# Kernel tuning notes

Measured on AMD Instinct MI355X. Metric: run time of the kernel, lower is better.

## Reference

```python
import jax, jax.numpy as jnp
import numpy as np

M, NN, D, H, DFF, L, EPG = 128, 62, 512, 8, 2048, 4, 600
K1, K2 = 50, 40  # ceil(0.8*62), ceil(0.8*50)
EPS = 1e-5


def _ln(x, g, b):
    mu = x.mean(-1, keepdims=True)
    v = x.var(-1, keepdims=True)
    return (x - mu) * jax.lax.rsqrt(v + EPS) * g + b


def _gcn(x, src, dst, mask, W, b, n):
    # PyG GCNConv: add self-loops, sym-normalized scatter-add aggregation
    h = x @ W
    w = mask.astype(x.dtype)
    deg = 1.0 + jax.ops.segment_sum(w, dst, num_segments=n)  # +1 self-loop
    dis = jax.lax.rsqrt(deg)
    coef = dis[src] * w * dis[dst]
    agg = jax.ops.segment_sum(coef[:, None] * h[src], dst, num_segments=n)
    return agg + h * (dis * dis)[:, None] + b  # second term = self-loop message


def _sagpool(x, src, dst, mask, Ws, bs, m, n_per, k):
    n = m * n_per
    score = _gcn(x, src, dst, mask, Ws, bs, n)[:, 0]
    _, topi = jax.lax.top_k(score.reshape(m, n_per), k)  # per-graph topk
    perm = (topi + jnp.arange(m)[:, None] * n_per).reshape(-1)
    xn = x[perm] * jnp.tanh(score[perm])[:, None]
    # filter_adj: keep edges with both endpoints surviving, remap indices
    nmap = jnp.full((n,), -1, jnp.int32).at[perm].set(jnp.arange(m * k, dtype=jnp.int32))
    ns, nd = nmap[src], nmap[dst]
    keep = mask & (ns >= 0) & (nd >= 0)
    return xn, jnp.where(keep, ns, 0), jnp.where(keep, nd, 0), keep


def _enc_layer(x, Wqkv, bqkv, Wo, bo, W1, b1, W2, b2, g1, be1, g2, be2):
    # post-norm TransformerEncoderLayer, relu activation, eval (no dropout)
    S, B, Dm = x.shape
    dh = Dm // H
    q, k, v = jnp.split(x @ Wqkv + bqkv, 3, axis=-1)
    q = q.reshape(S, B, H, dh)
    k = k.reshape(S, B, H, dh)
    v = v.reshape(S, B, H, dh)
    att = jnp.einsum('sbhd,tbhd->bhst', q, k) * (1.0 / np.sqrt(dh))
    o = jnp.einsum('bhst,tbhd->sbhd', jax.nn.softmax(att, axis=-1), v).reshape(S, B, Dm)
    x = _ln(x + o @ Wo + bo, g1, be1)
    f = jax.nn.relu(x @ W1 + b1) @ W2 + b2
    return _ln(x + f, g2, be2)


def _readout(h, m, k):
    hr = h.reshape(m, k, -1)
    return jnp.concatenate([hr.max(axis=1), hr.mean(axis=1)], axis=-1)  # gmp||gap


def _forward(edge_index, x, bn_g, bn_b, W_emb, enc_Wqkv, enc_bqkv, enc_Wo, enc_bo, enc_W1, enc_b1, enc_W2, enc_b2, enc_g1, enc_be1, enc_g2, enc_be2, W_emb1, conv1_W, conv1_b, convs_W, convs_b, pool1_W, pool1_b, pool2_W, pool2_b, fc1_W, fc1_b, fc2_W, fc2_b, fc3_W, fc3_b):
    m = x.shape[0] // NN
    xr = x.reshape(m, NN, NN)
    # BatchNorm1d(62) in training mode: per-channel stats over (N, L)
    mu = xr.mean(axis=(0, 2), keepdims=True)
    var = xr.var(axis=(0, 2), keepdims=True)
    xb = (xr - mu) * jax.lax.rsqrt(var + EPS) * bn_g[None, :, None] + bn_b[None, :, None]
    t = xb.transpose(1, 0, 2) @ W_emb  # [62, m, D] seq-first
    for l in range(L):
        t = _enc_layer(t, enc_Wqkv[l], enc_bqkv[l], enc_Wo[l], enc_bo[l], enc_W1[l], enc_b1[l], enc_W2[l], enc_b2[l], enc_g1[l], enc_be1[l], enc_g2[l], enc_be2[l])
    # faithful to torch: reshape [62,m,62] directly to [m*62,62] (no permute back)
    xg = (t @ W_emb1).reshape(m * NN, NN)
    src, dst = edge_index[0], edge_index[1]
    mask0 = jnp.ones(src.shape, bool)
    h = jax.nn.relu(_gcn(xg, src, dst, mask0, conv1_W, conv1_b, m * NN))
    h, s1, d1, m1 = _sagpool(h, src, dst, mask0, pool1_W, pool1_b, m, NN, K1)
    x1 = _readout(h, m, K1)
    for l in range(L - 1):
        h = jax.nn.relu(_gcn(h, s1, d1, m1, convs_W[l], convs_b[l], m * K1))
    h, s2, d2, m2 = _sagpool(h, s1, d1, m1, pool2_W, pool2_b, m, K1, K2)
    x2 = _readout(h, m, K2)
    z = x1 + x2
    z = jax.nn.relu(z @ fc1_W + fc1_b)
    z = jax.nn.relu(z @ fc2_W + fc2_b)
    return z @ fc3_W + fc3_b


def setup_inputs():
    key = jax.random.key(0)
    ki = iter(jax.random.split(key, 40))
    def nrm(shape, s=0.05):
        return jax.random.normal(next(ki), shape, jnp.float32) * s
    x = jax.random.normal(next(ki), (M * NN, NN), jnp.float32)
    off = jnp.arange(M, dtype=jnp.int32)[:, None] * NN
    src = jax.random.randint(next(ki), (M, EPG), 0, NN, dtype=jnp.int32) + off
    dst = jax.random.randint(next(ki), (M, EPG), 0, NN, dtype=jnp.int32) + off
    edge_index = jnp.stack([src.reshape(-1), dst.reshape(-1)])
    return dict(
        x=x, edge_index=edge_index,
        bn_g=jnp.ones(NN), bn_b=jnp.zeros(NN),
        W_emb=nrm((NN, D)),
        enc_Wqkv=nrm((L, D, 3 * D)), enc_bqkv=jnp.zeros((L, 3 * D)),
        enc_Wo=nrm((L, D, D)), enc_bo=jnp.zeros((L, D)),
        enc_W1=nrm((L, D, DFF)), enc_b1=jnp.zeros((L, DFF)),
        enc_W2=nrm((L, DFF, D)), enc_b2=jnp.zeros((L, D)),
        enc_g1=jnp.ones((L, D)), enc_be1=jnp.zeros((L, D)),
        enc_g2=jnp.ones((L, D)), enc_be2=jnp.zeros((L, D)),
        W_emb1=nrm((D, NN)),
        conv1_W=nrm((NN, D)), conv1_b=jnp.zeros(D),
        convs_W=nrm((L - 1, D, D)), convs_b=jnp.zeros((L - 1, D)),
        pool1_W=nrm((D, 1)), pool1_b=jnp.zeros(1),
        pool2_W=nrm((D, 1)), pool2_b=jnp.zeros(1),
        fc1_W=nrm((2 * D, D)), fc1_b=jnp.zeros(D),
        fc2_W=nrm((D, D // 2)), fc2_b=jnp.zeros(D // 2),
        fc3_W=nrm((D // 2, 2)), fc3_b=jnp.zeros(2))


def reference(x, edge_index, bn_g, bn_b, W_emb, enc_Wqkv, enc_bqkv, enc_Wo, enc_bo, enc_W1, enc_b1, enc_W2, enc_b2, enc_g1, enc_be1, enc_g2, enc_be2, W_emb1, conv1_W, conv1_b, convs_W, convs_b, pool1_W, pool1_b, pool2_W, pool2_b, fc1_W, fc1_b, fc2_W, fc2_b, fc3_W, fc3_b):
    return _forward(edge_index, x, bn_g, bn_b, W_emb, enc_Wqkv, enc_bqkv, enc_Wo, enc_bo, enc_W1, enc_b1, enc_W2, enc_b2, enc_g1, enc_be1, enc_g2, enc_be2, W_emb1, conv1_W, conv1_b, convs_W, convs_b, pool1_W, pool1_b, pool2_W, pool2_b, fc1_W, fc1_b, fc2_W, fc2_b, fc3_W, fc3_b)
```

## Files before the change

### kernel.cpp

```cpp
#include <hip/hip_runtime.h>
#include <float.h>
#include <math.h>

#define MG 128
#define NNODE 62
#define DD 512
#define NH 8
#define DH 64
#define DFF 2048
#define NLAYER 4
#define EPG 600
#define KP1 50
#define KP2 40
#define NTOK (MG*NNODE)
#define NEDGE (MG*EPG)
#define EPSV 1e-5f
#define PW 68

typedef unsigned short u16;
using bf16x8 = __attribute__((ext_vector_type(8))) short;
using f32x4  = __attribute__((ext_vector_type(4))) float;

__device__ __forceinline__ float wave_sum(float v) {
  for (int off = 32; off; off >>= 1) v += __shfl_xor(v, off);
  return v;
}
__device__ __forceinline__ float wave_max(float v) {
  for (int off = 32; off; off >>= 1) v = fmaxf(v, __shfl_xor(v, off));
  return v;
}
__device__ __forceinline__ u16 f2b(float x) {
  union { float f; unsigned u; } v; v.f = x;
  unsigned r = v.u + 0x7fffu + ((v.u >> 16) & 1u);
  return (u16)(r >> 16);
}
__device__ __forceinline__ float b2f(u16 h) {
  union { float f; unsigned u; } v; v.u = ((unsigned)h) << 16;
  return v.f;
}
__device__ __forceinline__ void f2bsplit(float x, u16& h, u16& l) {
  h = f2b(x);
  l = f2b(x - b2f(h));
}
__device__ __forceinline__ void load_lds16(const u16* g, u16* l) {
  __builtin_amdgcn_global_load_lds(
      (const __attribute__((address_space(1))) unsigned int*)(const void*)g,
      (__attribute__((address_space(3))) unsigned int*)(void*)l, 16, 0, 0);
}
__device__ __forceinline__ void cvt8(const float* __restrict__ p, bf16x8& vh, bf16x8& vl) {
  #pragma unroll
  for (int e = 0; e < 8; ++e) {
    u16 h, l; f2bsplit(p[e], h, l);
    vh[e] = (short)h; vl[e] = (short)l;
  }
}
__device__ __forceinline__ void cvt8s(const float* __restrict__ p, bf16x8& vh, bf16x8& vl) {
  #pragma unroll
  for (int e = 0; e < 8; ++e) {
    u16 h, l; f2bsplit(p[e*PW], h, l);
    vh[e] = (short)h; vl[e] = (short)l;
  }
}

__global__ __launch_bounds__(256) void bn_stats_kernel(const float* __restrict__ x,
    float* __restrict__ mu, float* __restrict__ rs) {
  int s = blockIdx.x;
  float sum = 0.f, sq = 0.f;
  for (int i = threadIdx.x; i < MG*NNODE; i += 256) {
    int b = i / NNODE, j = i - b*NNODE;
    float v = x[(size_t)(b*NNODE + s)*NNODE + j];
    sum += v; sq += v*v;
  }
  __shared__ float r1[4], r2[4];
  sum = wave_sum(sum); sq = wave_sum(sq);
  int wv = threadIdx.x >> 6, lane = threadIdx.x & 63;
  if (lane == 0) { r1[wv] = sum; r2[wv] = sq; }
  __syncthreads();
  if (threadIdx.x == 0) {
    float S = r1[0]+r1[1]+r1[2]+r1[3];
    float Q = r2[0]+r2[1]+r2[2]+r2[3];
    float m = S / (float)(MG*NNODE);
    float var = Q / (float)(MG*NNODE) - m*m;
    mu[s] = m;
    rs[s] = rsqrtf(var + EPSV);
  }
}

__global__ __launch_bounds__(256) void embed_kernel(const float* __restrict__ x,
    const float* __restrict__ mu, const float* __restrict__ rs,
    const float* __restrict__ gg, const float* __restrict__ bb,
    const float* __restrict__ W,
    u16* __restrict__ Th, u16* __restrict__ Tl) {
  int tok = blockIdx.x;
  int s = tok >> 7, b = tok & 127;
  __shared__ float xb[NNODE];
  if (threadIdx.x < NNODE) {
    float v = x[(size_t)(b*NNODE + s)*NNODE + threadIdx.x];
    xb[threadIdx.x] = (v - mu[s]) * rs[s] * gg[s] + bb[s];
  }
  __syncthreads();
  int d = threadIdx.x;
  float a0 = 0.f, a1 = 0.f;
  for (int j = 0; j < NNODE; ++j) {
    float xv = xb[j];
    a0 += xv * W[(size_t)j*DD + d];
    a1 += xv * W[(size_t)j*DD + d + 256];
  }
  size_t o = (size_t)tok*DD + d;
  u16 h, l;
  f2bsplit(a0, h, l); Th[o] = h; Tl[o] = l;
  f2bsplit(a1, h, l); Th[o+256] = h; Tl[o+256] = l;
}

__global__ __launch_bounds__(256) void gemm_kernel(const float* __restrict__ A,
    const float* __restrict__ B, float* __restrict__ C, int M, int N, int K) {
  __shared__ float As[16][68];
  __shared__ float Bs[16][68];
  int bm = blockIdx.y * 64, bn = blockIdx.x * 64;
  int tid = threadIdx.x;
  int tx = tid & 15, ty = tid >> 4;
  float acc[4][4] = {};
  for (int k0 = 0; k0 < K; k0 += 16) {
    {
      int row = tid >> 2; int kk = (tid & 3) * 4;
      int gm = bm + row;
      #pragma unroll
      for (int i = 0; i < 4; ++i) {
        int gk = k0 + kk + i;
        As[kk+i][row] = (gm < M && gk < K) ? A[(size_t)gm*K + gk] : 0.f;
      }
    }
    {
      int krow = tid >> 4; int nn = (tid & 15) * 4;
      int gk = k0 + krow;
      #pragma unroll
      for (int i = 0; i < 4; ++i) {
        int gn = bn + nn + i;
        Bs[krow][nn+i] = (gk < K && gn < N) ? B[(size_t)gk*N + gn] : 0.f;
      }
    }
    __syncthreads();
    #pragma unroll
    for (int k = 0; k < 16; ++k) {
      float a[4], bb2[4];
      #pragma unroll
      for (int i = 0; i < 4; ++i) a[i] = As[k][ty*4+i];
      #pragma unroll
      for (int j = 0; j < 4; ++j) bb2[j] = Bs[k][tx*4+j];
      #pragma unroll
      for (int i = 0; i < 4; ++i)
        #pragma unroll
        for (int j = 0; j < 4; ++j) acc[i][j] += a[i]*bb2[j];
    }
    __syncthreads();
  }
  #pragma unroll
  for (int i = 0; i < 4; ++i) {
    int gm = bm + ty*4 + i;
    if (gm >= M) continue;
    #pragma unroll
    for (int j = 0; j < 4; ++j) {
      int gn = bn + tx*4 + j;
      if (gn >= N) continue;
      C[(size_t)gm*N + gn] = acc[i][j];
    }
  }
}

__device__ __forceinline__ void transpose_split_tile(const float* __restrict__ W,
    u16* __restrict__ th, u16* __restrict__ tl,
    int K, int N, int Kp, int bx, int by, float (*t)[65]) {
  int k0 = by*64, n0 = bx*64;
  for (int i = threadIdx.x; i < 64*64; i += 256) {
    int r = i >> 6, c = i & 63;
    int gk = k0 + r, gn = n0 + c;
    t[r][c] = (gk < K && gn < N) ? W[(size_t)gk*N + gn] : 0.f;
  }
  __syncthreads();
  for (int i = threadIdx.x; i < 64*64; i += 256) {
    int r = i >> 6, c = i & 63;
    int gn = n0 + r, gk = k0 + c;
    u16 h, l; f2bsplit(t[c][r], h, l);
    th[(size_t)gn*Kp + gk] = h;
    tl[(size_t)gn*Kp + gk] = l;
  }
}

__global__ __launch_bounds__(256) void allT_kernel(
    const float* __restrict__ Wqkv, const float* __restrict__ Wo,
    const float* __restrict__ W1, const float* __restrict__ W2,
    u16* WQh, u16* WQl, u16* WOh, u16* WOl,
    u16* W1h, u16* W1l, u16* W2h, u16* W2l) {
  __shared__ float t[64][65];
  int layer = blockIdx.x / 768;
  int b = blockIdx.x % 768;
  const float* wqkv = Wqkv + (size_t)layer*DD*3*DD;
  const float* wo   = Wo   + (size_t)layer*DD*DD;
  const float* w1   = W1   + (size_t)layer*DD*DFF;
  const float* w2   = W2   + (size_t)layer*DFF*DD;
  size_t oq = (size_t)layer*1536*512, oo = (size_t)layer*512*512;
  size_t o1 = (size_t)layer*2048*512, o2 = (size_t)layer*512*2048;
  if (b < 192)      transpose_split_tile(wqkv, WQh+oq, WQl+oq, 512, 1536, 512, b % 24, b / 24, t);
  else if (b < 256) { int q = b - 192; transpose_split_tile(wo, WOh+oo, WOl+oo, 512, 512, 512, q % 8, q / 8, t); }
  else if (b < 512) { int q = b - 256; transpose_split_tile(w1, W1h+o1, W1l+o1, 512, 2048, 512, q % 32, q / 32, t); }
  else              { int q = b - 512; transpose_split_tile(w2, W2h+o2, W2l+o2, 2048, 512, 2048, q % 8, q / 8, t); }
}

__global__ __launch_bounds__(256) void gcnT_kernel(
    const float* __restrict__ WC, const float* __restrict__ convs_W,
    u16* CTh, u16* CTl, u16* CVh, u16* CVl) {
  __shared__ float t[64][65];
  int job = blockIdx.x >> 6, q = blockIdx.x & 63;
  int bx = q % 8, by = q / 8;
  if (job == 0) transpose_split_tile(WC, CTh, CTl, 512, 512, 512, bx, by, t);
  else {
    int l = job - 1;
    transpose_split_tile(convs_W + (size_t)l*DD*DD,
        CVh + (size_t)l*DD*DD, CVl + (size_t)l*DD*DD, 512, 512, 512, bx, by, t);
  }
}

template<bool RELU, int OUTMODE>
__global__ __launch_bounds__(256) void gemm3_kernel(
    const u16* __restrict__ Ah, const u16* __restrict__ Al,
    const u16* __restrict__ Bh, const u16* __restrict__ Bl,
    const float* __restrict__ bias,
    float* __restrict__ Cf, u16* __restrict__ Ch, u16* __restrict__ Cl,
    int Nreal, int Nstride, int Kp, int KC) {
  __shared__ alignas(16) u16 sA[2][2][4096];
  __shared__ alignas(16) u16 sB[2][2][4096];
  unsigned nx = gridDim.x, ny = gridDim.y;
  unsigned nwg = nx * ny * gridDim.z;
  unsigned lb = blockIdx.x + nx*(blockIdx.y + ny*blockIdx.z);
  unsigned swz = lb;
  if ((nwg & 7u) == 0u) {
    unsigned cpx = nwg >> 3;
    swz = (lb & 7u)*cpx + (lb >> 3);
  }
  unsigned bxi = swz % nx;
  unsigned rem = swz / nx;
  unsigned byi = rem % ny;
  unsigned bzi = rem / ny;
  int bm = byi * 128, bn = bxi * 128;
  int z = bzi;
  int tid = threadIdx.x;
  int wv = tid >> 6, lane = tid & 63;
  int wr = (wv >> 1) * 64, wc = (wv & 1) * 64;
  f32x4 acc[4][4];
  #pragma unroll
  for (int i = 0; i < 4; ++i)
    #pragma unroll
    for (int j = 0; j < 4; ++j) acc[i][j] = (f32x4){0.f,0.f,0.f,0.f};

  int r0 = tid >> 2;
  int lin = (tid & 3) * 8;
  int c0 = lin ^ (((r0 >> 1) & 3) << 3);
  int r1 = r0 + 64;
  int c1 = lin ^ (((r1 >> 1) & 3) << 3);
  int fr = lane & 15, fo = (lane >> 4) * 8;

  int kbeg = z * KC;
  const u16* pA0 = Ah + (size_t)(bm + r0)*Kp + kbeg + c0;
  const u16* pA1 = Ah + (size_t)(bm + r1)*Kp + kbeg + c1;
  const u16* pB0 = Bh + (size_t)(bn + r0)*Kp + kbeg + c0;
  const u16* pB1 = Bh + (size_t)(bn + r1)*Kp + kbeg + c1;
  const ptrdiff_t dA = Al - Ah;
  const ptrdiff_t dB = Bl - Bh;

  auto stage = [&](int bi) {
    load_lds16(pA0,      &sA[bi][0][tid*8]);
    load_lds16(pA1,      &sA[bi][0][2048 + tid*8]);
    load_lds16(pA0 + dA, &sA[bi][1][tid*8]);
    load_lds16(pA1 + dA, &sA[bi][1][2048 + tid*8]);
    load_lds16(pB0,      &sB[bi][0][tid*8]);
    load_lds16(pB1,      &sB[bi][0][2048 + tid*8]);
    load_lds16(pB0 + dB, &sB[bi][1][tid*8]);
    load_lds16(pB1 + dB, &sB[bi][1][2048 + tid*8]);
    pA0 += 32; pA1 += 32; pB0 += 32; pB1 += 32;
  };

  int nk = KC >> 5;
  stage(0);
  int cur = 0;
  for (int t = 0; t < nk; ++t) {
    if (t + 1 < nk) {
      stage(cur ^ 1);
      asm volatile("s_waitcnt vmcnt(8)" ::: "memory");
    } else {
      asm volatile("s_waitcnt vmcnt(0)" ::: "memory");
    }
    __builtin_amdgcn_s_barrier();
    __builtin_amdgcn_sched_barrier(0);
    bf16x8 ah[4], al[4], bh[4], bl[4];
    #pragma unroll
    for (int i = 0; i < 4; ++i) {
      int ra = wr + i*16 + fr;
      int ea = ra*32 + (fo ^ (((ra >> 1) & 3) << 3));
      ah[i] = *(const bf16x8*)&sA[cur][0][ea];
      al[i] = *(const bf16x8*)&sA[cur][1][ea];
      int rb = wc + i*16 + fr;
      int eb = rb*32 + (fo ^ (((rb >> 1) & 3) << 3));
      bh[i] = *(const bf16x8*)&sB[cur][0][eb];
      bl[i] = *(const bf16x8*)&sB[cur][1][eb];
    }
    #pragma unroll
    for (int i = 0; i < 4; ++i)
      #pragma unroll
      for (int j = 0; j < 4; ++j) {
        acc[i][j] = __builtin_amdgcn_mfma_f32_16x16x32_bf16(ah[i], bh[j], acc[i][j], 0, 0, 0);
        acc[i][j] = __builtin_amdgcn_mfma_f32_16x16x32_bf16(ah[i], bl[j], acc[i][j], 0, 0, 0);
        acc[i][j] = __builtin_amdgcn_mfma_f32_16x16x32_bf16(al[i], bh[j], acc[i][j], 0, 0, 0);
      }
    __builtin_amdgcn_s_barrier();
    cur ^= 1;
  }
  size_t pstride = (size_t)gridDim.y * 128 * Nstride;
  int cr = (lane >> 4) * 4, cc = lane & 15;
  #pragma unroll
  for (int i = 0; i < 4; ++i) {
    #pragma unroll
    for (int j = 0; j < 4; ++j) {
      int gn = bn + wc + j*16 + cc;
      if (gn >= Nstride) continue;
      #pragma unroll
      for (int q = 0; q < 4; ++q) {
        int gm = bm + wr + i*16 + cr + q;
        float v = acc[i][j][q];
        if (gn < Nreal) { if (bias && z == 0) v += bias[gn]; } else v = 0.f;
        if (RELU) v = fmaxf(v, 0.f);
        if (OUTMODE == 0) {
          Cf[(size_t)z*pstride + (size_t)gm*Nstride + gn] = v;
        } else if (OUTMODE == 1) {
          size_t o = (size_t)z*pstride + (size_t)gm*Nstride + gn;
          u16 h, l; f2bsplit(v, h, l);
          Ch[o] = h; Cl[o] = l;
        } else {
          int which = gn >> 9, hh2 = (gn >> 6) & 7, d = gn & 63;
          int b2 = gm & 127, s2 = gm >> 7;
          Cf[(size_t)((which*NH + hh2)*MG + b2)*4096 + s2*64 + d] = v;
        }
      }
    }
  }
}

__global__ __launch_bounds__(256) void attn_kernel(const float* __restrict__ QKV,
    u16* __restrict__ Oh, u16* __restrict__ Ol) {
  int b = blockIdx.x >> 3, h = blockIdx.x & 7;
  __shared__ float sQ[64*PW];
  __shared__ float sK[64*PW];
  __shared__ float sV[64*PW];
  u16* sPh = (u16*)sK;
  u16* sPl = ((u16*)sK) + 4096;
  float* Ss = sQ;
  int tid = threadIdx.x, wv = tid >> 6, lane = tid & 63;
  int fr = lane & 15, fq = lane >> 4;
  size_t base0 = (size_t)(h*MG + b)*4096;
  const float* Qg = QKV + base0;
  const float* Kg = QKV + (size_t)NH*MG*4096 + base0;
  const float* Vg = QKV + (size_t)2*NH*MG*4096 + base0;
  #pragma unroll
  for (int i = 0; i < 4; ++i) {
    int c = tid + i*256;
    int r = c >> 4, col = (c & 15) * 4;
    f32x4 q4 = *(const f32x4*)(Qg + (size_t)c*4);
    f32x4 k4 = *(const f32x4*)(Kg + (size_t)c*4);
    f32x4 v4 = *(const f32x4*)(Vg + (size_t)c*4);
    *(f32x4*)&sQ[r*PW + col] = q4;
    *(f32x4*)&sK[r*PW + col] = k4;
    *(f32x4*)&sV[r*PW + col] = v4;
  }
  if (tid < 128) sV[(62 + (tid >> 6))*PW + (tid & 63)] = 0.f;
  __syncthreads();
  int rA = 16*wv + fr;
  bf16x8 qh[2], ql[2];
  #pragma unroll
  for (int kk = 0; kk < 2; ++kk)
    cvt8(&sQ[rA*PW + 32*kk + 8*fq], qh[kk], ql[kk]);
  __syncthreads();
  f32x4 accS[4];
  #pragma unroll
  for (int j = 0; j < 4; ++j) accS[j] = (f32x4){0.f,0.f,0.f,0.f};
  __builtin_amdgcn_s_setprio(1);
  #pragma unroll
  for (int kk = 0; kk < 2; ++kk) {
    #pragma unroll
    for (int j = 0; j < 4; ++j) {
      int rB = 16*j + fr;
      bf16x8 kh, kl;
      cvt8(&sK[rB*PW + 32*kk + 8*fq], kh, kl);
      accS[j] = __builtin_amdgcn_mfma_f32_16x16x32_bf16(qh[kk], kh, accS[j], 0, 0, 0);
      accS[j] = __builtin_amdgcn_mfma_f32_16x16x32_bf16(qh[kk], kl, accS[j], 0, 0, 0);
      accS[j] = __builtin_amdgcn_mfma_f32_16x16x32_bf16(ql[kk], kh, accS[j], 0, 0, 0);
    }
  }
  __builtin_amdgcn_s_setprio(0);
  #pragma unroll
  for (int j = 0; j < 4; ++j)
    #pragma unroll
    for (int q = 0; q < 4; ++q)
      Ss[(16*wv + fq*4 + q)*PW + 16*j + fr] = accS[j][q];
  __syncthreads();
  for (int rr = 0; rr < 16; ++rr) {
    int row = 16*wv + rr;
    float sv = (lane < NNODE) ? Ss[row*PW + lane]*0.125f : -FLT_MAX;
    float mx = wave_max(sv);
    float e = (lane < NNODE) ? expf(sv - mx) : 0.f;
    float sm = wave_sum(e);
    float p = e / sm;
    u16 ph, pl; f2bsplit(p, ph, pl);
    int pos = row*64 + ((((lane >> 3) ^ (row & 7)) << 3) | (lane & 7));
    sPh[pos] = ph; sPl[pos] = pl;
  }
  __syncthreads();
  f32x4 accO[4];
  #pragma unroll
  for (int j = 0; j < 4; ++j) accO[j] = (f32x4){0.f,0.f,0.f,0.f};
  __builtin_amdgcn_s_setprio(1);
  #pragma unroll
  for (int kk = 0; kk < 2; ++kk) {
    int cha = (((4*kk + fq) ^ (rA & 7)) << 3);
    bf16x8 pah = *(const bf16x8*)&sPh[rA*64 + cha];
    bf16x8 pal = *(const bf16x8*)&sPl[rA*64 + cha];
    #pragma unroll
    for (int j = 0; j < 4; ++j) {
      bf16x8 vh, vl;
      cvt8s(&sV[(32*kk + 8*fq)*PW + 16*j + fr], vh, vl);
      accO[j] = __builtin_amdgcn_mfma_f32_16x16x32_bf16(pah, vh, accO[j], 0, 0, 0);
      accO[j] = __builtin_amdgcn_mfma_f32_16x16x32_bf16(pah, vl, accO[j], 0, 0, 0);
      accO[j] = __builtin_amdgcn_mfma_f32_16x16x32_bf16(pal, vh, accO[j], 0, 0, 0);
    }
  }
  __builtin_amdgcn_s_setprio(0);
  #pragma unroll
  for (int j = 0; j < 4; ++j) {
    #pragma unroll
    for (int q = 0; q < 4; ++q) {
      int s2 = 16*wv + fq*4 + q;
      if (s2 < NNODE) {
        int d = 16*j + fr;
        size_t o = ((size_t)(s2*MG + b))*DD + h*DH + d;
        u16 hh2, ll2; f2bsplit(accO[j][q], hh2, ll2);
        Oh[o] = hh2; Ol[o] = ll2;
      }
    }
  }
}

__global__ __launch_bounds__(256) void add_ln_kernel(
    u16* __restrict__ Xh, u16* __restrict__ Xl,
    const float* __restrict__ P, int nchunk,
    const float* __restrict__ gg, const float* __restrict__ bb) {
  size_t row = blockIdx.x;
  int t = threadIdx.x;
  const size_t MN = (size_t)NTOK*DD;
  float r0 = 0.f, r1 = 0.f;
  for (int z = 0; z < nchunk; ++z) {
    r0 += P[z*MN + row*DD + t];
    r1 += P[z*MN + row*DD + t + 256];
  }
  float v0 = b2f(Xh[row*DD + t]) + b2f(Xl[row*DD + t]) + r0;
  float v1 = b2f(Xh[row*DD + t + 256]) + b2f(Xl[row*DD + t + 256]) + r1;
  __shared__ float red[4];
  float s = wave_sum(v0 + v1);
  int wv = t >> 6, lane = t & 63;
  if (lane == 0) red[wv] = s;
  __syncthreads();
  float mu = (red[0]+red[1]+red[2]+red[3]) * (1.f/DD);
  float d0 = v0 - mu, d1 = v1 - mu;
  float q = wave_sum(d0*d0 + d1*d1);
  __syncthreads();
  if (lane == 0) red[wv] = q;
  __syncthreads();
  float var = (red[0]+red[1]+red[2]+red[3]) * (1.f/DD);
  float rs = rsqrtf(var + EPSV);
  float o0 = d0*rs*gg[t] + bb[t];
  float o1 = d1*rs*gg[t+256] + bb[t+256];
  u16 h, l;
  f2bsplit(o0, h, l); Xh[row*DD + t] = h; Xl[row*DD + t] = l;
  f2bsplit(o1, h, l); Xh[row*DD + t+256] = h; Xl[row*DD + t+256] = l;
}

__global__ void fill_int_kernel(int* p, int v, int n) {
  int i = blockIdx.x*256 + threadIdx.x;
  if (i < n) p[i] = v;
}
__global__ void zero_f_kernel(float* p, int n) {
  int i = blockIdx.x*256 + threadIdx.x;
  if (i < n) p[i] = 0.f;
}
__global__ void count_deg_kernel(const int* __restrict__ dst, int* deg, int n) {
  int e = blockIdx.x*256 + threadIdx.x;
  if (e < n) atomicAdd(&deg[dst[e]], 1);
}
__global__ void dis_kernel(const int* __restrict__ deg, float* dis, int n) {
  int i = blockIdx.x*256+threadIdx.x;
  if (i < n) dis[i] = rsqrtf((float)deg[i]);
}
__global__ void coef0_kernel(const int* __restrict__ src, const int* __restrict__ dst,
                             const float* __restrict__ dis, float* coef) {
  int e = blockIdx.x*256+threadIdx.x;
  if (e < NEDGE) coef[e] = dis[src[e]]*dis[dst[e]];
}
__global__ void coef1_kernel(const int* __restrict__ src, const int* __restrict__ dst,
                             const int* __restrict__ keep,
                             const float* __restrict__ dis, float* coef) {
  int e = blockIdx.x*256+threadIdx.x;
  if (e < NEDGE) coef[e] = keep[e] ? dis[src[e]]*dis[dst[e]] : 0.f;
}

__global__ __launch_bounds__(64) void diagA_kernel(const float* __restrict__ dis,
    float* __restrict__ AG, int NP) {
  int g = blockIdx.x, lane = threadIdx.x;
  if (lane < NP) {
    float d = dis[g*NP + lane];
    AG[(size_t)g*4096 + lane*64 + lane] = d*d;
  }
}
__global__ __launch_bounds__(256) void edgeA_kernel(const int* __restrict__ src,
    const int* __restrict__ dst, const float* __restrict__ coef,
    float* __restrict__ AG, int NP) {
  int e = blockIdx.x*256 + threadIdx.x;
  if (e >= NEDGE) return;
  float c = coef[e];
  if (c == 0.f) return;
  int g = e / EPG;
  int ls = src[e] - g*NP, ld = dst[e] - g*NP;
  atomicAdd(&AG[(size_t)g*4096 + ld*64 + ls], c);
}

__global__ __launch_bounds__(256) void dense_agg_kernel(
    const float* __restrict__ AG,
    const float* __restrict__ P, int nchunk, size_t mn,
    const float* __restrict__ bias,
    float* __restrict__ Hout, int NP, int relu,
    u16* __restrict__ outh, u16* __restrict__ outl) {
  int g = blockIdx.x >> 3;
  int ct = (blockIdx.x & 7) * 64;
  __shared__ float hls[64*64];
  __shared__ float At[64*68];
  int base = g * NP;
  for (int idx = threadIdx.x; idx < 64*64; idx += 256) {
    int r = idx >> 6, c = idx & 63;
    float v = 0.f;
    if (r < NP) {
      for (int z = 0; z < nchunk; ++z)
        v += P[z*mn + (size_t)(base+r)*DD + ct + c];
    }
    hls[idx] = v;
    At[c*68 + r] = AG[(size_t)g*4096 + idx];
  }
  __syncthreads();
  int wv = threadIdx.x >> 6, lane = threadIdx.x & 63;
  int i0 = wv * 16;
  f32x4 acc[4];
  #pragma unroll
  for (int q = 0; q < 4; ++q) acc[q] = (f32x4){0.f,0.f,0.f,0.f};
  for (int j = 0; j < NP; ++j) {
    float hv = hls[j*64 + lane];
    const f32x4* ap = (const f32x4*)&At[j*68 + i0];
    f32x4 a0 = ap[0], a1 = ap[1], a2 = ap[2], a3 = ap[3];
    #pragma unroll
    for (int t = 0; t < 4; ++t) {
      acc[0][t] += a0[t] * hv;
      acc[1][t] += a1[t] * hv;
      acc[2][t] += a2[t] * hv;
      acc[3][t] += a3[t] * hv;
    }
  }
  float bv = bias[ct + lane];
  #pragma unroll
  for (int q = 0; q < 4; ++q) {
    #pragma unroll
    for (int t = 0; t < 4; ++t) {
      int i = i0 + q*4 + t;
      if (i < NP) {
        float v = acc[q][t] + bv;
        if (relu) v = fmaxf(v, 0.f);
        size_t o = (size_t)(base+i)*DD + ct + lane;
        Hout[o] = v;
        if (outh) { u16 h, l; f2bsplit(v, h, l); outh[o] = h; outl[o] = l; }
      }
    }
  }
}

__global__ __launch_bounds__(64) void dense_score_kernel(
    const float* __restrict__ AG, const float* __restrict__ hsv,
    const float* __restrict__ pb, float* __restrict__ sc, int NP) {
  int g = blockIdx.x, lane = threadIdx.x;
  __shared__ float hls[64];
  __shared__ float At[64*65];
  hls[lane] = (lane < NP) ? hsv[g*NP + lane] : 0.f;
  for (int idx = lane; idx < 64*64; idx += 64) {
    int i = idx >> 6, j = idx & 63;
    At[j*65 + i] = AG[(size_t)g*4096 + idx];
  }
  __syncthreads();
  if (lane < NP) {
    float acc = 0.f;
    for (int j = 0; j < NP; ++j) acc += At[j*65 + lane] * hls[j];
    sc[g*NP + lane] = acc + pb[0];
  }
}

__global__ __launch_bounds__(256) void gemv_kernel(const float* __restrict__ h,
    const float* __restrict__ wv, float* __restrict__ out, int n) {
  int node = blockIdx.x*4 + (threadIdx.x >> 6);
  int lane = threadIdx.x & 63;
  if (node >= n) return;
  const float* row = h + (size_t)node*DD;
  float acc = 0.f;
  for (int d = lane; d < DD; d += 64) acc += row[d]*wv[d];
  acc = wave_sum(acc);
  if (lane == 0) out[node] = acc;
}

__global__ __launch_bounds__(64) void topk_kernel(const float* __restrict__ sc,
    int* __restrict__ perm, int NP, int KK) {
  int g = blockIdx.x, lane = threadIdx.x;
  float v = (lane < NP) ? sc[g*NP+lane] : -FLT_MAX;
  for (int r = 0; r < KK; ++r) {
    float bv = v; int bi = lane;
    for (int off = 32; off; off >>= 1) {
      float ov = __shfl_xor(bv, off);
      int oi = __shfl_xor(bi, off);
      if (ov > bv || (ov == bv && oi < bi)) { bv = ov; bi = oi; }
    }
    if (lane == 0) perm[g*KK + r] = bi;
    if (lane == bi) v = -FLT_MAX;
  }
}

__global__ __launch_bounds__(256) void gather_kernel(const float* __restrict__ h,
    const float* __restrict__ sc, const int* __restrict__ perm,
    float* __restrict__ xn, u16* __restrict__ outh, u16* __restrict__ outl,
    int NP, int KK) {
  int j = blockIdx.x;
  int g = j / KK;
  int pi = perm[j];
  float t = tanhf(sc[g*NP + pi]);
  const float* srow = h + (size_t)(g*NP + pi)*DD;
  size_t o = (size_t)j*DD + threadIdx.x;
  float v0 = srow[threadIdx.x]*t;
  float v1 = srow[threadIdx.x+256]*t;
  xn[o] = v0; xn[o+256] = v1;
  if (outh) {
    u16 hh, ll;
    f2bsplit(v0, hh, ll); outh[o] = hh; outl[o] = ll;
    f2bsplit(v1, hh, ll); outh[o+256] = hh; outl[o+256] = ll;
  }
}

__global__ void nmap_scatter_kernel(const int* __restrict__ perm, int* __restrict__ nmap) {
  int j = blockIdx.x*256 + threadIdx.x;
  if (j < MG*KP1) nmap[(j/KP1)*NNODE + perm[j]] = j;
}

__global__ void filter_kernel(const int* __restrict__ src0, const int* __restrict__ dst0,
    const int* __restrict__ nmap, int* __restrict__ es, int* __restrict__ ed,
    int* __restrict__ keep, int* __restrict__ deg1) {
  int e = blockIdx.x*256+threadIdx.x;
  if (e >= NEDGE) return;
  int ns = nmap[src0[e]], nd = nmap[dst0[e]];
  int k = (ns >= 0) && (nd >= 0);
  es[e] = k ? ns : 0;
  ed[e] = k ? nd : 0;
  keep[e] = k;
  if (k) atomicAdd(&deg1[nd], 1);
}

__global__ __launch_bounds__(256) void readout_kernel(const float* __restrict__ h,
    float* __restrict__ z, int KK, int acc) {
  int g = blockIdx.x;
  for (int c = threadIdx.x; c < DD; c += 256) {
    float mx = -FLT_MAX, sm = 0.f;
    for (int r = 0; r < KK; ++r) {
      float v = h[(size_t)(g*KK+r)*DD + c];
      mx = fmaxf(mx, v); sm += v;
    }
    float mean = sm / (float)KK;
    if (acc) { z[(size_t)g*1024 + c] += mx; z[(size_t)g*1024 + 512 + c] += mean; }
    else     { z[(size_t)g*1024 + c]  = mx; z[(size_t)g*1024 + 512 + c]  = mean; }
  }
}

__global__ __launch_bounds__(256) void mlp1_kernel(const float* __restrict__ Z,
    const float* __restrict__ W1, float* __restrict__ Pm) {
  int b = blockIdx.x;
  int g = b >> 2, zc = b & 3;
  __shared__ float z[256];
  int t = threadIdx.x;
  z[t] = Z[(size_t)g*1024 + zc*256 + t];
  __syncthreads();
  const float* Wb = W1 + (size_t)zc*256*512;
  float a0 = 0.f, a1 = 0.f;
  for (int k = 0; k < 256; ++k) {
    float zv = z[k];
    a0 += zv * Wb[(size_t)k*512 + t];
    a1 += zv * Wb[(size_t)k*512 + t + 256];
  }
  size_t o = ((size_t)zc*MG + g)*512;
  Pm[o + t] = a0;
  Pm[o + t + 256] = a1;
}

__global__ __launch_bounds__(256) void mlp2_kernel(const float* __restrict__ Pm,
    const float* __restrict__ b1,
    const float* __restrict__ W2, const float* __restrict__ b2,
    const float* __restrict__ W3, const float* __restrict__ b3,
    float* __restrict__ out) {
  int g = blockIdx.x;
  int t = threadIdx.x;
  int wv = t >> 6, lane = t & 63;
  __shared__ float h1[512];
  __shared__ float p2[4][256];
  __shared__ float h2[256];
  #pragma unroll
  for (int half = 0; half < 2; ++half) {
    int n = t + half*256;
    float a = b1[n];
    #pragma unroll
    for (int zc = 0; zc < 4; ++zc) a += Pm[((size_t)zc*MG + g)*512 + n];
    h1[n] = fmaxf(a, 0.f);
  }
  __syncthreads();
  {
    float a[4] = {0.f, 0.f, 0.f, 0.f};
    for (int k = wv*128; k < wv*128 + 128; ++k) {
      float hv = h1[k];
      #pragma unroll
      for (int q = 0; q < 4; ++q)
        a[q] += hv * W2[(size_t)k*256 + lane + q*64];
    }
    #pragma unroll
    for (int q = 0; q < 4; ++q) p2[wv][lane + q*64] = a[q];
  }
  __syncthreads();
  h2[t] = fmaxf(p2[0][t] + p2[1][t] + p2[2][t] + p2[3][t] + b2[t], 0.f);
  __syncthreads();
  if (wv < 2) {
    float acc = 0.f;
    for (int k = lane; k < 256; k += 64) acc += h2[k]*W3[(size_t)k*2 + wv];
    acc = wave_sum(acc);
    if (lane == 0) out[(size_t)g*2 + wv] = acc + b3[wv];
  }
}

extern "C" void kernel_launch(void* const* d_in, const int* in_sizes, int n_in,
                              void* d_out, int out_size, void* d_ws, size_t ws_size,
                              hipStream_t stream) {
  const float* x       = (const float*)d_in[0];
  const int*   edge    = (const int*)d_in[1];
  const float* bn_g    = (const float*)d_in[2];
  const float* bn_b    = (const float*)d_in[3];
  const float* W_emb   = (const float*)d_in[4];
  const float* Wqkv    = (const float*)d_in[5];
  const float* bqkv    = (const float*)d_in[6];
  const float* Wo      = (const float*)d_in[7];
  const float* bo      = (const float*)d_in[8];
  const float* W1      = (const float*)d_in[9];
  const float* b1      = (const float*)d_in[10];
  const float* W2      = (const float*)d_in[11];
  const float* b2      = (const float*)d_in[12];
  const float* g1      = (const float*)d_in[13];
  const float* be1     = (const float*)d_in[14];
  const float* g2      = (const float*)d_in[15];
  const float* be2     = (const float*)d_in[16];
  const float* W_emb1  = (const float*)d_in[17];
  const float* conv1_W = (const float*)d_in[18];
  const float* conv1_b = (const float*)d_in[19];
  const float* convs_W = (const float*)d_in[20];
  const float* convs_b = (const float*)d_in[21];
  const float* pool1_W = (const float*)d_in[22];
  const float* pool1_b = (const float*)d_in[23];
  const float* pool2_W = (const float*)d_in[24];
  const float* pool2_b = (const float*)d_in[25];
  const float* fc1_W   = (const float*)d_in[26];
  const float* fc1_b   = (const float*)d_in[27];
  const float* fc2_W   = (const float*)d_in[28];
  const float* fc2_b   = (const float*)d_in[29];
  const float* fc3_W   = (const float*)d_in[30];
  const float* fc3_b   = (const float*)d_in[31];
  (void)in_sizes; (void)n_in; (void)out_size; (void)ws_size;

  const int* srcp = edge;
  const int* dstp = edge + NEDGE;

  char* wsb = (char*)d_ws;
  size_t off = 0;
  auto alloc = [&](size_t bytes)->void* {
    void* p = wsb + off;
    off += (bytes + 255) & ~(size_t)255;
    return p;
  };
  const size_t MN = (size_t)NTOK*DD;
  size_t qkvB = (size_t)3*NH*MG*4096*4, ffnB = (size_t)NTOK*DFF*2*2;
  char* BIGU  = (char*)alloc(qkvB > ffnB ? qkvB : ffnB);
  u16* BIGh   = (u16*)BIGU;
  u16* BIGl   = BIGh + (size_t)NTOK*DFF;
  float* QKVf = (float*)BIGU;
  float* PART = (float*)alloc(4*MN*4);
  u16* Th   = (u16*)alloc(MN*2);
  u16* Tl   = (u16*)alloc(MN*2);
  u16* ATh  = (u16*)alloc(MN*2);
  u16* ATl  = (u16*)alloc(MN*2);
  u16* Hh   = (u16*)alloc((size_t)MG*KP1*DD*2);
  u16* Hl   = (u16*)alloc((size_t)MG*KP1*DD*2);
  u16* WQh  = (u16*)alloc((size_t)4*1536*512*2);
  u16* WQl  = (u16*)alloc((size_t)4*1536*512*2);
  u16* WOh  = (u16*)alloc((size_t)4*512*512*2);
  u16* WOl  = (u16*)alloc((size_t)4*512*512*2);
  u16* W1h  = (u16*)alloc((size_t)4*2048*512*2);
  u16* W1l  = (u16*)alloc((size_t)4*2048*512*2);
  u16* W2h  = (u16*)alloc((size_t)4*512*2048*2);
  u16* W2l  = (u16*)alloc((size_t)4*512*2048*2);
  float* WCf = (float*)alloc((size_t)512*512*4);
  u16* CTh  = (u16*)alloc((size_t)512*512*2);
  u16* CTl  = (u16*)alloc((size_t)512*512*2);
  u16* CVh  = (u16*)alloc((size_t)3*512*512*2);
  u16* CVl  = (u16*)alloc((size_t)3*512*512*2);
  float* AG0 = (float*)alloc((size_t)MG*4096*4);
  float* AG1 = (float*)alloc((size_t)MG*4096*4);
  float* MU   = (float*)alloc(NNODE*4);
  float* RS   = (float*)alloc(NNODE*4);
  int*   DEG0 = (int*)alloc(NTOK*4);
  float* DIS0 = (float*)alloc(NTOK*4);
  float* COEF0= (float*)alloc(NEDGE*4);
  float* HS   = (float*)alloc(NTOK*4);
  float* SC   = (float*)alloc(NTOK*4);
  int*   PERM1= (int*)alloc(MG*KP1*4);
  int*   NMAP = (int*)alloc(NTOK*4);
  int*   ES1  = (int*)alloc(NEDGE*4);
  int*   ED1  = (int*)alloc(NEDGE*4);
  int*   KEEP1= (int*)alloc(NEDGE*4);
  int*   DEG1 = (int*)alloc(MG*KP1*4);
  float* DIS1 = (float*)alloc(MG*KP1*4);
  float* COEF1= (float*)alloc(NEDGE*4);
  int*   PERM2= (int*)alloc(MG*KP2*4);
  float* Z    = (float*)alloc(MG*1024*4);
  float* Pm   = (float*)alloc((size_t)4*MG*512*4);

  float* PA = PART;
  float* PB = PART + 2*MN;

  bn_stats_kernel<<<NNODE, 256, 0, stream>>>(x, MU, RS);
  embed_kernel<<<NTOK, 256, 0, stream>>>(x, MU, RS, bn_g, bn_b, W_emb, Th, Tl);
  allT_kernel<<<4*768, 256, 0, stream>>>(Wqkv, Wo, W1, W2,
      WQh, WQl, WOh, WOl, W1h, W1l, W2h, W2l);
  fill_int_kernel<<<(NTOK+255)/256, 256, 0, stream>>>(DEG0, 1, NTOK);
  count_deg_kernel<<<(NEDGE+255)/256, 256, 0, stream>>>(dstp, DEG0, NEDGE);
  dis_kernel<<<(NTOK+255)/256, 256, 0, stream>>>(DEG0, DIS0, NTOK);
  coef0_kernel<<<(NEDGE+255)/256, 256, 0, stream>>>(srcp, dstp, DIS0, COEF0);
  zero_f_kernel<<<(MG*4096+255)/256, 256, 0, stream>>>(AG0, MG*4096);
  diagA_kernel<<<MG, 64, 0, stream>>>(DIS0, AG0, NNODE);
  edgeA_kernel<<<(NEDGE+255)/256, 256, 0, stream>>>(srcp, dstp, COEF0, AG0, NNODE);
  gemm_kernel<<<dim3(8,8), 256, 0, stream>>>(W_emb1, conv1_W, WCf, 512, 512, NNODE);
  gcnT_kernel<<<256, 256, 0, stream>>>(WCf, convs_W, CTh, CTl, CVh, CVl);

  for (int l = 0; l < NLAYER; ++l) {
    size_t oq = (size_t)l*1536*512, oo = (size_t)l*512*512;
    size_t o1 = (size_t)l*2048*512, o2 = (size_t)l*512*2048;
    gemm3_kernel<false,2><<<dim3(12,62,1), 256, 0, stream>>>(Th, Tl, WQh+oq, WQl+oq,
        bqkv + (size_t)l*3*DD, QKVf, nullptr, nullptr, 3*DD, 3*DD, DD, DD);
    attn_kernel<<<MG*NH, 256, 0, stream>>>(QKVf, ATh, ATl);
    gemm3_kernel<false,0><<<dim3(4,62,2), 256, 0, stream>>>(ATh, ATl, WOh+oo, WOl+oo,
        bo + (size_t)l*DD, PART, nullptr, nullptr, DD, DD, DD, 256);
    add_ln_kernel<<<NTOK, 256, 0, stream>>>(Th, Tl, PART, 2,
        g1 + (size_t)l*DD, be1 + (size_t)l*DD);
    gemm3_kernel<true,1><<<dim3(16,62,1), 256, 0, stream>>>(Th, Tl, W1h+o1, W1l+o1,
        b1 + (size_t)l*DFF, nullptr, BIGh, BIGl, DFF, DFF, DD, DD);
    gemm3_kernel<false,0><<<dim3(4,62,2), 256, 0, stream>>>(BIGh, BIGl, W2h+o2, W2l+o2,
        b2 + (size_t)l*DD, PART, nullptr, nullptr, DD, DD, DFF, 1024);
    add_ln_kernel<<<NTOK, 256, 0, stream>>>(Th, Tl, PART, 2,
        g2 + (size_t)l*DD, be2 + (size_t)l*DD);
  }

  gemm3_kernel<false,0><<<dim3(4,62,2), 256, 0, stream>>>(Th, Tl, CTh, CTl,
      nullptr, PA, nullptr, nullptr, DD, DD, DD, 256);
  dense_agg_kernel<<<MG*8, 256, 0, stream>>>(AG0, PA, 2, MN, conv1_b,
      PA, NNODE, 1, nullptr, nullptr);

  gemv_kernel<<<(NTOK+3)/4, 256, 0, stream>>>(PA, pool1_W, HS, NTOK);
  dense_score_kernel<<<MG, 64, 0, stream>>>(AG0, HS, pool1_b, SC, NNODE);
  topk_kernel<<<MG, 64, 0, stream>>>(SC, PERM1, NNODE, KP1);
  gather_kernel<<<MG*KP1, 256, 0, stream>>>(PA, SC, PERM1, PA + MN, Hh, Hl, NNODE, KP1);
  readout_kernel<<<MG, 256, 0, stream>>>(PA + MN, Z, KP1, 0);

  fill_int_kernel<<<(NTOK+255)/256, 256, 0, stream>>>(NMAP, -1, NTOK);
  nmap_scatter_kernel<<<(MG*KP1+255)/256, 256, 0, stream>>>(PERM1, NMAP);
  fill_int_kernel<<<(MG*KP1+255)/256, 256, 0, stream>>>(DEG1, 1, MG*KP1);
  filter_kernel<<<(NEDGE+255)/256, 256, 0, stream>>>(srcp, dstp, NMAP, ES1, ED1, KEEP1, DEG1);
  dis_kernel<<<(MG*KP1+255)/256, 256, 0, stream>>>(DEG1, DIS1, MG*KP1);
  coef1_kernel<<<(NEDGE+255)/256, 256, 0, stream>>>(ES1, ED1, KEEP1, DIS1, COEF1);
  zero_f_kernel<<<(MG*4096+255)/256, 256, 0, stream>>>(AG1, MG*4096);
  diagA_kernel<<<MG, 64, 0, stream>>>(DIS1, AG1, KP1);
  edgeA_kernel<<<(NEDGE+255)/256, 256, 0, stream>>>(ES1, ED1, COEF1, AG1, KP1);

  const size_t MNP = (size_t)MG*KP1*DD;
  float* bases[3] = { PB, PA, PB };
  float* hfin = nullptr;
  for (int l = 0; l < NLAYER-1; ++l) {
    float* Pb = bases[l];
    gemm3_kernel<false,0><<<dim3(4,50,2), 256, 0, stream>>>(Hh, Hl, CVh + (size_t)l*DD*DD,
        CVl + (size_t)l*DD*DD, nullptr, Pb, nullptr, nullptr, DD, DD, DD, 256);
    dense_agg_kernel<<<MG*8, 256, 0, stream>>>(AG1, Pb, 2, MNP, convs_b + (size_t)l*DD,
        Pb, KP1, 1, (l < NLAYER-2) ? Hh : nullptr, (l < NLAYER-2) ? Hl : nullptr);
    hfin = Pb;
  }

  gemv_kernel<<<(MG*KP1+3)/4, 256, 0, stream>>>(hfin, pool2_W, HS, MG*KP1);
  dense_score_kernel<<<MG, 64, 0, stream>>>(AG1, HS, pool2_b, SC, KP1);
  topk_kernel<<<MG, 64, 0, stream>>>(SC, PERM2, KP1, KP2);
  gather_kernel<<<MG*KP2, 256, 0, stream>>>(hfin, SC, PERM2, PA, nullptr, nullptr, KP1, KP2);
  readout_kernel<<<MG, 256, 0, stream>>>(PA, Z, KP2, 1);

  mlp1_kernel<<<MG*4, 256, 0, stream>>>(Z, fc1_W, Pm);
  mlp2_kernel<<<MG, 256, 0, stream>>>(Pm, fc1_b, fc2_W, fc2_b, fc3_W, fc3_b, (float*)d_out);
}
```

Before: 1.618 ms.

## Widen split-bf16 GEMM tile to 128x256 and generalize XCD swizzle

Doubles the N extent of each gemm3 workgroup tile from 128 to 256. Each wave now computes 64x128 with 32 accumulators, and B-fragments are loaded per column inside the MFMA loop so each one is reused across the four A fragments. Grid x dimensions are halved to match. The XCD swizzle now also handles workgroup counts that are not multiples of 8. The change aims for more MFMA work per LDS byte and fewer workgroups, but it doubles the B LDS footprint and raises register pressure (launch_bounds 256,1), which may lower occupancy.

```diff
diff --git a/kernel.cpp b/kernel.cpp
--- a/kernel.cpp
+++ b/kernel.cpp
@@ -221,49 +221,49 @@
 }
 
 template<bool RELU, int OUTMODE>
-__global__ __launch_bounds__(256) void gemm3_kernel(
+__global__ __launch_bounds__(256, 1) void gemm3_kernel(
     const u16* __restrict__ Ah, const u16* __restrict__ Al,
     const u16* __restrict__ Bh, const u16* __restrict__ Bl,
     const float* __restrict__ bias,
     float* __restrict__ Cf, u16* __restrict__ Ch, u16* __restrict__ Cl,
     int Nreal, int Nstride, int Kp, int KC) {
   __shared__ alignas(16) u16 sA[2][2][4096];
-  __shared__ alignas(16) u16 sB[2][2][4096];
+  __shared__ alignas(16) u16 sB[2][2][8192];
   unsigned nx = gridDim.x, ny = gridDim.y;
   unsigned nwg = nx * ny * gridDim.z;
   unsigned lb = blockIdx.x + nx*(blockIdx.y + ny*blockIdx.z);
-  unsigned swz = lb;
-  if ((nwg & 7u) == 0u) {
-    unsigned cpx = nwg >> 3;
-    swz = (lb & 7u)*cpx + (lb >> 3);
-  }
+  unsigned qd = nwg >> 3, rm = nwg & 7u;
+  unsigned xcd = lb & 7u, idx = lb >> 3;
+  unsigned basep = (xcd < rm) ? xcd*(qd+1) : rm*(qd+1) + (xcd-rm)*qd;
+  unsigned swz = basep + idx;
   unsigned bxi = swz % nx;
   unsigned rem = swz / nx;
   unsigned byi = rem % ny;
   unsigned bzi = rem / ny;
-  int bm = byi * 128, bn = bxi * 128;
+  int bm = byi * 128, bn = bxi * 256;
   int z = bzi;
   int tid = threadIdx.x;
   int wv = tid >> 6, lane = tid & 63;
-  int wr = (wv >> 1) * 64, wc = (wv & 1) * 64;
-  f32x4 acc[4][4];
+  int wr = (wv >> 1) * 64, wc = (wv & 1) * 128;
+  f32x4 acc[4][8];
   #pragma unroll
   for (int i = 0; i < 4; ++i)
     #pragma unroll
-    for (int j = 0; j < 4; ++j) acc[i][j] = (f32x4){0.f,0.f,0.f,0.f};
+    for (int j = 0; j < 8; ++j) acc[i][j] = (f32x4){0.f,0.f,0.f,0.f};
 
   int r0 = tid >> 2;
   int lin = (tid & 3) * 8;
-  int c0 = lin ^ (((r0 >> 1) & 3) << 3);
-  int r1 = r0 + 64;
-  int c1 = lin ^ (((r1 >> 1) & 3) << 3);
   int fr = lane & 15, fo = (lane >> 4) * 8;
 
   int kbeg = z * KC;
-  const u16* pA0 = Ah + (size_t)(bm + r0)*Kp + kbeg + c0;
-  const u16* pA1 = Ah + (size_t)(bm + r1)*Kp + kbeg + c1;
-  const u16* pB0 = Bh + (size_t)(bn + r0)*Kp + kbeg + c0;
-  const u16* pB1 = Bh + (size_t)(bn + r1)*Kp + kbeg + c1;
+  int cA0 = lin ^ (((r0 >> 1) & 3) << 3);
+  int cA1 = lin ^ ((((r0+64) >> 1) & 3) << 3);
+  const u16* pA0 = Ah + (size_t)(bm + r0)*Kp + kbeg + cA0;
+  const u16* pA1 = Ah + (size_t)(bm + r0 + 64)*Kp + kbeg + cA1;
+  const u16* pB0 = Bh + (size_t)(bn + r0)*Kp + kbeg + cA0;
+  const u16* pB1 = Bh + (size_t)(bn + r0 + 64)*Kp + kbeg + cA1;
+  const u16* pB2 = Bh + (size_t)(bn + r0 + 128)*Kp + kbeg + cA0;
+  const u16* pB3 = Bh + (size_t)(bn + r0 + 192)*Kp + kbeg + cA1;
   const ptrdiff_t dA = Al - Ah;
   const ptrdiff_t dB = Bl - Bh;
 
@@ -274,9 +274,13 @@
     load_lds16(pA1 + dA, &sA[bi][1][2048 + tid*8]);
     load_lds16(pB0,      &sB[bi][0][tid*8]);
     load_lds16(pB1,      &sB[bi][0][2048 + tid*8]);
+    load_lds16(pB2,      &sB[bi][0][4096 + tid*8]);
+    load_lds16(pB3,      &sB[bi][0][6144 + tid*8]);
     load_lds16(pB0 + dB, &sB[bi][1][tid*8]);
     load_lds16(pB1 + dB, &sB[bi][1][2048 + tid*8]);
-    pA0 += 32; pA1 += 32; pB0 += 32; pB1 += 32;
+    load_lds16(pB2 + dB, &sB[bi][1][4096 + tid*8]);
+    load_lds16(pB3 + dB, &sB[bi][1][6144 + tid*8]);
+    pA0 += 32; pA1 += 32; pB0 += 32; pB1 += 32; pB2 += 32; pB3 += 32;
   };
 
   int nk = KC >> 5;
@@ -285,32 +289,33 @@
   for (int t = 0; t < nk; ++t) {
     if (t + 1 < nk) {
       stage(cur ^ 1);
-      asm volatile("s_waitcnt vmcnt(8)" ::: "memory");
+      asm volatile("s_waitcnt vmcnt(12)" ::: "memory");
     } else {
       asm volatile("s_waitcnt vmcnt(0)" ::: "memory");
     }
     __builtin_amdgcn_s_barrier();
     __builtin_amdgcn_sched_barrier(0);
-    bf16x8 ah[4], al[4], bh[4], bl[4];
+    bf16x8 ah[4], al[4];
     #pragma unroll
     for (int i = 0; i < 4; ++i) {
       int ra = wr + i*16 + fr;
       int ea = ra*32 + (fo ^ (((ra >> 1) & 3) << 3));
       ah[i] = *(const bf16x8*)&sA[cur][0][ea];
       al[i] = *(const bf16x8*)&sA[cur][1][ea];
-      int rb = wc + i*16 + fr;
+    }
+    #pragma unroll
+    for (int j = 0; j < 8; ++j) {
+      int rb = wc + j*16 + fr;
       int eb = rb*32 + (fo ^ (((rb >> 1) & 3) << 3));
-      bh[i] = *(const bf16x8*)&sB[cur][0][eb];
-      bl[i] = *(const bf16x8*)&sB[cur][1][eb];
-    }
-    #pragma unroll
-    for (int i = 0; i < 4; ++i)
+      bf16x8 bh = *(const bf16x8*)&sB[cur][0][eb];
+      bf16x8 bl = *(const bf16x8*)&sB[cur][1][eb];
       #pragma unroll
-      for (int j = 0; j < 4; ++j) {
-        acc[i][j] = __builtin_amdgcn_mfma_f32_16x16x32_bf16(ah[i], bh[j], acc[i][j], 0, 0, 0);
-        acc[i][j] = __builtin_amdgcn_mfma_f32_16x16x32_bf16(ah[i], bl[j], acc[i][j], 0, 0, 0);
-        acc[i][j] = __builtin_amdgcn_mfma_f32_16x16x32_bf16(al[i], bh[j], acc[i][j], 0, 0, 0);
+      for (int i = 0; i < 4; ++i) {
+        acc[i][j] = __builtin_amdgcn_mfma_f32_16x16x32_bf16(ah[i], bh, acc[i][j], 0, 0, 0);
+        acc[i][j] = __builtin_amdgcn_mfma_f32_16x16x32_bf16(ah[i], bl, acc[i][j], 0, 0, 0);
+        acc[i][j] = __builtin_amdgcn_mfma_f32_16x16x32_bf16(al[i], bh, acc[i][j], 0, 0, 0);
       }
+    }
     __builtin_amdgcn_s_barrier();
     cur ^= 1;
   }
@@ -319,7 +324,7 @@
   #pragma unroll
   for (int i = 0; i < 4; ++i) {
     #pragma unroll
-    for (int j = 0; j < 4; ++j) {
+    for (int j = 0; j < 8; ++j) {
       int gn = bn + wc + j*16 + cc;
       if (gn >= Nstride) continue;
       #pragma unroll
@@ -861,22 +866,22 @@
   for (int l = 0; l < NLAYER; ++l) {
     size_t oq = (size_t)l*1536*512, oo = (size_t)l*512*512;
     size_t o1 = (size_t)l*2048*512, o2 = (size_t)l*512*2048;
-    gemm3_kernel<false,2><<<dim3(12,62,1), 256, 0, stream>>>(Th, Tl, WQh+oq, WQl+oq,
+    gemm3_kernel<false,2><<<dim3(6,62,1), 256, 0, stream>>>(Th, Tl, WQh+oq, WQl+oq,
         bqkv + (size_t)l*3*DD, QKVf, nullptr, nullptr, 3*DD, 3*DD, DD, DD);
     attn_kernel<<<MG*NH, 256, 0, stream>>>(QKVf, ATh, ATl);
-    gemm3_kernel<false,0><<<dim3(4,62,2), 256, 0, stream>>>(ATh, ATl, WOh+oo, WOl+oo,
+    gemm3_kernel<false,0><<<dim3(2,62,2), 256, 0, stream>>>(ATh, ATl, WOh+oo, WOl+oo,
         bo + (size_t)l*DD, PART, nullptr, nullptr, DD, DD, DD, 256);
     add_ln_kernel<<<NTOK, 256, 0, stream>>>(Th, Tl, PART, 2,
         g1 + (size_t)l*DD, be1 + (size_t)l*DD);
-    gemm3_kernel<true,1><<<dim3(16,62,1), 256, 0, stream>>>(Th, Tl, W1h+o1, W1l+o1,
+    gemm3_kernel<true,1><<<dim3(8,62,1), 256, 0, stream>>>(Th, Tl, W1h+o1, W1l+o1,
         b1 + (size_t)l*DFF, nullptr, BIGh, BIGl, DFF, DFF, DD, DD);
-    gemm3_kernel<false,0><<<dim3(4,62,2), 256, 0, stream>>>(BIGh, BIGl, W2h+o2, W2l+o2,
+    gemm3_kernel<false,0><<<dim3(2,62,2), 256, 0, stream>>>(BIGh, BIGl, W2h+o2, W2l+o2,
         b2 + (size_t)l*DD, PART, nullptr, nullptr, DD, DD, DFF, 1024);
     add_ln_kernel<<<NTOK, 256, 0, stream>>>(Th, Tl, PART, 2,
         g2 + (size_t)l*DD, be2 + (size_t)l*DD);
   }
 
-  gemm3_kernel<false,0><<<dim3(4,62,2), 256, 0, stream>>>(Th, Tl, CTh, CTl,
+  gemm3_kernel<false,0><<<dim3(2,62,2), 256, 0, stream>>>(Th, Tl, CTh, CTl,
       nullptr, PA, nullptr, nullptr, DD, DD, DD, 256);
   dense_agg_kernel<<<MG*8, 256, 0, stream>>>(AG0, PA, 2, MN, conv1_b,
       PA, NNODE, 1, nullptr, nullptr);
@@ -902,7 +907,7 @@
   float* hfin = nullptr;
   for (int l = 0; l < NLAYER-1; ++l) {
     float* Pb = bases[l];
-    gemm3_kernel<false,0><<<dim3(4,50,2), 256, 0, stream>>>(Hh, Hl, CVh + (size_t)l*DD*DD,
+    gemm3_kernel<false,0><<<dim3(2,50,2), 256, 0, stream>>>(Hh, Hl, CVh + (size_t)l*DD*DD,
         CVl + (size_t)l*DD*DD, nullptr, Pb, nullptr, nullptr, DD, DD, DD, 256);
     dense_agg_kernel<<<MG*8, 256, 0, stream>>>(AG1, Pb, 2, MNP, convs_b + (size_t)l*DD,
         Pb, KP1, 1, (l < NLAYER-2) ? Hh : nullptr, (l < NLAYER-2) ? Hl : nullptr);
```

New measurement: 2.049 ms. 26.7% more time.
